# Kernel optimization log

Hardware: AMD Instinct MI355X
Metric: run time of the kernel (lower is better)

## Reference

```python
import jax, jax.numpy as jnp
import numpy as np

QMIN, QMAX = -128.0, 127.0


def setup_inputs() -> dict:
    key = jax.random.key(0)
    k1, k2, k3 = jax.random.split(key, 3)
    x = jax.random.normal(k1, (8, 32, 32, 32), jnp.float32)          # NCHW
    weight = jax.random.normal(k2, (32, 32, 3, 3), jnp.float32) * 0.1  # OIHW
    bias = jax.random.normal(k3, (32,), jnp.float32) * 0.01
    # lut[i, j] = (i - 128) * (j - 128), indexed by (q + 128).
    i = jnp.arange(256, dtype=jnp.float32) - 128.0
    lut = i[:, None] * i[None, :]
    return {"x": x, "weight": weight, "bias": bias, "lut": lut}


def reference(x, weight, bias, lut):
    # dynamic per-tensor scales (qmethod = ('dynamic','tensor','tensor'))
    sf = jax.lax.stop_gradient(jnp.max(jnp.abs(x)) / 127.0)
    sw = jax.lax.stop_gradient(jnp.max(jnp.abs(weight)) / 127.0)

    qx = jnp.clip(jnp.round(x / sf), QMIN, QMAX)        # int8 values as float
    qw = jnp.clip(jnp.round(weight / sw), QMIN, QMAX)

    # STE fake-quant tensors (forward = dequant, backward = identity)
    x_fq = x + jax.lax.stop_gradient(qx * sf - x)
    w_fq = weight + jax.lax.stop_gradient(qw * sw - weight)

    pad = ((1, 1), (1, 1))
    conv_fq = jax.lax.conv_general_dilated(
        x_fq, w_fq, window_strides=(1, 1), padding=pad,
        dimension_numbers=('NCHW', 'OIHW', 'NCHW'))

    # ---- LUT-based int8 conv path (forward value) ----
    # im2col on the int8 activation codes; zero padding -> q=0 -> index 128,
    # and lut[128, :] == 0, matching zero-padded conv.
    patches = jax.lax.conv_general_dilated_patches(
        qx, filter_shape=(3, 3), window_strides=(1, 1), padding=pad)
    N, K, Hp, Wp = patches.shape                       # K = Cin*kh*kw
    O = qw.shape[0]
    ix = (patches + 128.0).astype(jnp.int32).reshape(N, K, Hp * Wp)
    ix = jnp.transpose(ix, (0, 2, 1))                  # [N, P, K]
    iw = (qw.reshape(O, K) + 128.0).astype(jnp.int32)  # [O, K]

    # gather approximate products and accumulate over the window
    prods = lut[ix[:, :, None, :], iw[None, None, :, :]]  # [N, P, O, K]
    out_lut = (sf * sw) * jnp.sum(prods, axis=-1)          # [N, P, O]
    out_lut = jnp.transpose(out_lut, (0, 2, 1)).reshape(N, O, Hp, Wp)

    b = bias[None, :, None, None]
    out_fq = conv_fq + b
    out_lut = out_lut + b
    # forward returns the LUT result; gradients flow through the fake-quant conv (STE)
    return out_fq + jax.lax.stop_gradient(out_lut - out_fq)
```

## Files before the change

### kernel.cpp

```cpp
#include <hip/hip_runtime.h>

#define W_N 9216

static __device__ __forceinline__ int dot4(int a, int b, int acc) {
#if defined(__has_builtin)
#if __has_builtin(__builtin_amdgcn_sdot4)
  return __builtin_amdgcn_sdot4(a, b, acc, false);
#define DOT4_DONE 1
#endif
#endif
#ifndef DOT4_DONE
  #pragma unroll
  for (int k = 0; k < 4; k++)
    acc += ((a >> (8*k)) << 24 >> 24) * ((b >> (8*k)) << 24 >> 24);
  return acc;
#endif
}

__global__ __launch_bounds__(256) void k_scales(
    const float4* __restrict__ x4, const float4* __restrict__ w4,
    int* __restrict__ xmax_bits, float* __restrict__ sw_out,
    signed char* __restrict__ qw_r) {
  __shared__ float red[256];
  __shared__ float s_sw;
  int b = blockIdx.x, t = threadIdx.x;
  float m = 0.f;
  if (b < 64) {
    #pragma unroll
    for (int k = 0; k < 4; k++) {
      float4 v = x4[b * 1024 + k * 256 + t];
      m = fmaxf(m, fmaxf(fmaxf(fabsf(v.x), fabsf(v.y)), fmaxf(fabsf(v.z), fabsf(v.w))));
    }
  } else {
    for (int i = t; i < W_N / 4; i += 256) {
      float4 v = w4[i];
      m = fmaxf(m, fmaxf(fmaxf(fabsf(v.x), fabsf(v.y)), fmaxf(fabsf(v.z), fabsf(v.w))));
    }
  }
  red[t] = m;
  __syncthreads();
  #pragma unroll
  for (int s = 128; s >= 1; s >>= 1) {
    if (t < s) red[t] = fmaxf(red[t], red[t + s]);
    __syncthreads();
  }
  if (b < 64) {
    if (t == 0) atomicMax(xmax_bits, __float_as_int(red[0]));
    return;
  }
  if (t == 0) {
    float sw = red[0] / 127.f;
    sw_out[0] = sw;
    s_sw = sw;
  }
  __syncthreads();
  float sw = s_sw;
  const float* w = (const float*)w4;
  for (int i = t; i < W_N; i += 256) {
    int o = i / 288, rem = i % 288;
    int c = rem / 9, k9 = rem % 9;
    float r = rintf(w[i] / sw);
    r = fminf(fmaxf(r, -128.f), 127.f);
    qw_r[(o * 9 + k9) * 32 + c] = (signed char)(int)r;
  }
}

__global__ __launch_bounds__(256, 4) void k_conv(
    const float* __restrict__ x, const signed char* __restrict__ qw_r,
    const float* __restrict__ bias, const int* __restrict__ xmax_bits,
    const float* __restrict__ sw_in, float* __restrict__ out) {
  int b = blockIdx.x;
  int strip = b & 3;
  int o = (b >> 2) & 31;
  int n = b >> 7;
  int t = threadIdx.x;

  __shared__ int ts[8 * 10 * 34];

  float sf = __int_as_float(xmax_bits[0]) / 127.f;
  float inv_sf = 1.f / sf;
  const float* xn = x + n * 32768;

  for (int idx = t; idx < 2720; idx += 256) {
    int g = idx / 340, s = idx % 340;
    int r = s / 34, cc = s % 34;
    int gh = strip * 8 - 1 + r;
    int gw = cc - 1;
    int packed = 0;
    if ((unsigned)gh < 32u && (unsigned)gw < 32u) {
      const float* p = xn + g * 4096 + gh * 32 + gw;
      #pragma unroll
      for (int j = 0; j < 4; j++) {
        float r1 = fminf(fmaxf(rintf(p[j * 1024] * inv_sf), -128.f), 127.f);
        packed |= ((int)r1 & 0xff) << (8 * j);
      }
    }
    ts[idx] = packed;
  }
  __syncthreads();

  int row = t >> 5, col = t & 31;
  const int* wq = (const int*)qw_r + o * 72;

  int acc = 0;
  #pragma unroll
  for (int g = 0; g < 8; g++) {
    const int* tg = ts + g * 340;
    #pragma unroll
    for (int ky = 0; ky < 3; ky++) {
      const int* tr = tg + (row + ky) * 34 + col;
      acc = dot4(tr[0], wq[(ky * 3 + 0) * 8 + g], acc);
      acc = dot4(tr[1], wq[(ky * 3 + 1) * 8 + g], acc);
      acc = dot4(tr[2], wq[(ky * 3 + 2) * 8 + g], acc);
    }
  }

  float scale = sf * sw_in[0];
  int h = strip * 8 + row;
  out[(n * 32 + o) * 1024 + h * 32 + col] = scale * (float)acc + bias[o];
}

extern "C" void kernel_launch(void* const* d_in, const int* in_sizes, int n_in,
                              void* d_out, int out_size, void* d_ws, size_t ws_size,
                              hipStream_t stream) {
  const float* x    = (const float*)d_in[0];
  const float* w    = (const float*)d_in[1];
  const float* bias = (const float*)d_in[2];
  float* out = (float*)d_out;

  char* wsb = (char*)d_ws;
  int*         xmax_bits = (int*)(wsb + 0);
  float*       sw_out    = (float*)(wsb + 64);
  signed char* qw_r      = (signed char*)(wsb + 2048);

  k_scales<<<65, 256, 0, stream>>>((const float4*)x, (const float4*)w,
                                   xmax_bits, sw_out, qw_r);
  k_conv<<<1024, 256, 0, stream>>>(x, qw_r, bias, xmax_bits, sw_out, out);
}
```

Before: 78.71 us.

## Compute eight output channels per block reusing register-cached input patches

Each block now computes 8 output channels instead of 1. It loads its 72 packed input words into registers once and reuses them across the channels, with two accumulators to split the dependency chain. This removes the redundant per-channel quantization and shared-memory staging of the input tile, which was repeated 32 times before. In exchange the grid shrinks from 1024 to 128 blocks, which risks underfilling the GPU, and register pressure rises now that the occupancy hint is dropped.

```diff
diff --git a/kernel.cpp b/kernel.cpp
--- a/kernel.cpp
+++ b/kernel.cpp
@@ -65,17 +65,17 @@
   }
 }
 
-__global__ __launch_bounds__(256, 4) void k_conv(
+__global__ __launch_bounds__(256) void k_conv(
     const float* __restrict__ x, const signed char* __restrict__ qw_r,
     const float* __restrict__ bias, const int* __restrict__ xmax_bits,
     const float* __restrict__ sw_in, float* __restrict__ out) {
   int b = blockIdx.x;
-  int strip = b & 3;
-  int o = (b >> 2) & 31;
-  int n = b >> 7;
+  int og = b & 3;
+  int strip = (b >> 2) & 3;
+  int n = b >> 4;
   int t = threadIdx.x;
 
-  __shared__ int ts[8 * 10 * 34];
+  __shared__ int ts[8 * 340];
 
   float sf = __int_as_float(xmax_bits[0]) / 127.f;
   float inv_sf = 1.f / sf;
@@ -100,24 +100,37 @@
   __syncthreads();
 
   int row = t >> 5, col = t & 31;
-  const int* wq = (const int*)qw_r + o * 72;
 
-  int acc = 0;
+  int p[9][8];
   #pragma unroll
-  for (int g = 0; g < 8; g++) {
-    const int* tg = ts + g * 340;
+  for (int ky = 0; ky < 3; ky++)
     #pragma unroll
-    for (int ky = 0; ky < 3; ky++) {
-      const int* tr = tg + (row + ky) * 34 + col;
-      acc = dot4(tr[0], wq[(ky * 3 + 0) * 8 + g], acc);
-      acc = dot4(tr[1], wq[(ky * 3 + 1) * 8 + g], acc);
-      acc = dot4(tr[2], wq[(ky * 3 + 2) * 8 + g], acc);
-    }
-  }
+    for (int kx = 0; kx < 3; kx++)
+      #pragma unroll
+      for (int g = 0; g < 8; g++)
+        p[ky * 3 + kx][g] = ts[g * 340 + (row + ky) * 34 + (col + kx)];
 
   float scale = sf * sw_in[0];
   int h = strip * 8 + row;
-  out[(n * 32 + o) * 1024 + h * 32 + col] = scale * (float)acc + bias[o];
+  float* outn = out + n * 32768 + h * 32 + col;
+
+  for (int oi = 0; oi < 8; oi++) {
+    int o = og * 8 + oi;
+    const int* wr = (const int*)qw_r + o * 72;
+    int a0 = 0, a1 = 0;
+    #pragma unroll
+    for (int pos = 0; pos < 9; pos++) {
+      a0 = dot4(p[pos][0], wr[pos * 8 + 0], a0);
+      a1 = dot4(p[pos][1], wr[pos * 8 + 1], a1);
+      a0 = dot4(p[pos][2], wr[pos * 8 + 2], a0);
+      a1 = dot4(p[pos][3], wr[pos * 8 + 3], a1);
+      a0 = dot4(p[pos][4], wr[pos * 8 + 4], a0);
+      a1 = dot4(p[pos][5], wr[pos * 8 + 5], a1);
+      a0 = dot4(p[pos][6], wr[pos * 8 + 6], a0);
+      a1 = dot4(p[pos][7], wr[pos * 8 + 7], a1);
+    }
+    outn[o * 1024] = scale * (float)(a0 + a1) + bias[o];
+  }
 }
 
 extern "C" void kernel_launch(void* const* d_in, const int* in_sizes, int n_in,
@@ -135,5 +148,5 @@
 
   k_scales<<<65, 256, 0, stream>>>((const float4*)x, (const float4*)w,
                                    xmax_bits, sw_out, qw_r);
-  k_conv<<<1024, 256, 0, stream>>>(x, qw_r, bias, xmax_bits, sw_out, out);
+  k_conv<<<128, 256, 0, stream>>>(x, qw_r, bias, xmax_bits, sw_out, out);
 }
```

Measured after the change: 84.94 us. 1.08x slower.
